# Optimization experiments

Measured on AMD Instinct MI355X. Metric: run time of the kernel, lower is better.

The kernel has to match this reference:

```python
import jax, jax.numpy as jnp
import numpy as np

B, L, C = 16, 450, 768
MID = 256
K = 8912
TEMP = 0.07
ENT_TEMP = 0.01
EPS_NORM = 1e-12


def _l2norm(v):
    n = jnp.sqrt(jnp.sum(v * v, axis=-1, keepdims=True))
    return v / jnp.maximum(n, EPS_NORM)


def setup_inputs() -> dict:
    key = jax.random.key(0)
    k1, k2, k3, k4 = jax.random.split(key, 4)
    x = jax.random.normal(k1, (B, L, C), dtype=jnp.float32)
    W_down = jax.random.normal(k2, (C, MID), dtype=jnp.float32) * (1.0 / np.sqrt(C))
    b_down = jnp.zeros((MID,), dtype=jnp.float32)
    bound = 1.0 / np.sqrt(MID)
    embedding = jax.random.uniform(k3, (K, MID), dtype=jnp.float32, minval=-bound, maxval=bound)
    return {"x": x, "W_down": W_down, "b_down": b_down, "embedding": embedding}


def reference(x, W_down, b_down, embedding):
    Bx, Lx, Cx = x.shape
    # down projection: [B,L,C] -> [B,L,MID]
    z = jnp.einsum('blc,cm->blm', x, W_down) + b_down
    zf = z.reshape(Bx * Lx, MID)
    zn = _l2norm(zf)                       # [N, MID]
    en = _l2norm(embedding)                # [K, MID]
    # squared euclidean distance on the unit sphere: ||a-b||^2 = 2 - 2 a.b
    d = 2.0 - 2.0 * jnp.einsum('nm,km->nk', zn, en)   # [N, K]
    idx = jnp.argmin(d, axis=1)            # [N]
    # codebook usage (no-grad stats)
    occ = jnp.bincount(idx, length=K)
    code_book_usage = jnp.mean((occ > 0).astype(jnp.float32))
    # soft assignment probs (hard_quant branch)
    logits = -d / TEMP
    probs = jax.nn.softmax(logits, axis=1)
    z_q = en[idx]                          # [N, MID]
    vq_loss = jnp.mean((z_q - jax.lax.stop_gradient(zn)) ** 2)
    commit_loss = jnp.mean((jax.lax.stop_gradient(z_q) - zn) ** 2)
    # straight-through estimator
    z_q_ste = zn + jax.lax.stop_gradient(z_q - zn)
    # entropy loss on affinity = -d at entropy temperature
    fa = -d / ENT_TEMP
    p = jax.nn.softmax(fa, axis=-1)
    lp = jax.nn.log_softmax(fa, axis=-1)
    avg_probs = jnp.mean(p, axis=0)
    avg_entropy = -jnp.sum(avg_probs * jnp.log(avg_probs + 1e-5))
    sample_entropy = -jnp.mean(jnp.sum(p * lp, axis=-1))
    entropy_loss = sample_entropy - avg_entropy
    return (z_q_ste.reshape(Bx, Lx, MID), probs.reshape(Bx, Lx, K),
            code_book_usage, vq_loss, commit_loss, entropy_loss)
```

## Files before the change

### kernel.cpp

```cpp
#include <hip/hip_runtime.h>
#include <stdint.h>

#define N_TOK 7200
#define N_PAD 7232
#define N_PAD_A 7296
#define K_CODE 8912
#define K_PAD 8960
#define N_KT 140
#define NKT128 70
#define NMT128 57
#define MID 256
#define C_DIM 768
#define INV_TEMP (1.0f/0.07f)
#define INV_ETEMP 100.0f
#define MARGIN 0.02f
#define CAND_CAP 64
#define EPS_N 1e-12f

typedef __attribute__((ext_vector_type(8))) short short8;
typedef __attribute__((ext_vector_type(4))) float f32x4;

__device__ __forceinline__ unsigned short f2bf(float f) {
    unsigned u = __float_as_uint(f);
    u += 0x7fffu + ((u >> 16) & 1u);
    return (unsigned short)(u >> 16);
}
__device__ __forceinline__ float bf2f(unsigned short h) {
    return __uint_as_float(((unsigned)h) << 16);
}

__device__ __forceinline__ void gload16(const void* g, void* l) {
    __builtin_amdgcn_global_load_lds(
        (const __attribute__((address_space(1))) unsigned int*)g,
        (__attribute__((address_space(3))) unsigned int*)l,
        16, 0, 0);
}

__global__ void k_init(float* ap_acc, int* used, float* acc4, int* ccnt,
                       unsigned short* zn_h, unsigned short* en_h) {
    int i = blockIdx.x * 256 + threadIdx.x;
    if (i < K_CODE) { ap_acc[i] = 0.f; used[i] = 0; }
    if (i < N_TOK) ccnt[i] = 0;
    if (i < 4) acc4[i] = 0.f;
    for (int j = i; j < (N_PAD_A - N_TOK) * MID; j += 8960) zn_h[(size_t)N_TOK * MID + j] = 0;
    for (int j = i; j < (K_PAD - K_CODE) * MID; j += 8960) en_h[(size_t)K_CODE * MID + j] = 0;
}

__global__ void k_wsplit(const float* __restrict__ W,
                         unsigned short* __restrict__ wt_h,
                         unsigned short* __restrict__ wt_l) {
    int i = blockIdx.x * 256 + threadIdx.x;
    if (i >= C_DIM * MID) return;
    int c = i / MID, t = i % MID;
    float v = W[i];
    unsigned short h = f2bf(v);
    unsigned short l = f2bf(v - bf2f(h));
    wt_h[t * C_DIM + c] = h;
    wt_l[t * C_DIM + c] = l;
}

__global__ void k_ennorm(const float* __restrict__ emb,
                         float* __restrict__ en,
                         unsigned short* __restrict__ en_h) {
    int n = blockIdx.x, t = threadIdx.x;
    float v = emb[n * MID + t];
    __shared__ float sb[256];
    sb[t] = v * v; __syncthreads();
    for (int s = 128; s > 0; s >>= 1) { if (t < s) sb[t] += sb[t + s]; __syncthreads(); }
    float nn = sqrtf(sb[0]);
    float o = v / fmaxf(nn, EPS_N);
    en[n * MID + t] = o;
    en_h[n * MID + t] = f2bf(o);
}

__global__ __launch_bounds__(256) void k_zgemm(const float* __restrict__ x,
                                               const unsigned short* __restrict__ wt_h,
                                               const unsigned short* __restrict__ wt_l,
                                               float* __restrict__ zbuf) {
    __shared__ unsigned short ls[4 * 64 * 72];
    unsigned short* xh = ls;
    unsigned short* xl = ls + 64 * 72;
    unsigned short* wh = ls + 2 * 64 * 72;
    unsigned short* wl = ls + 3 * 64 * 72;
    int tid = threadIdx.x;
    int m0 = blockIdx.y * 64;
    int t0 = blockIdx.x * 64;
    int lane = tid & 63, wv = tid >> 6;
    int quad = lane >> 4, l15 = lane & 15;
    int mrow0 = (wv >> 1) * 32, ncol0 = (wv & 1) * 32;
    f32x4 acc[2][2] = {};

    for (int ch = 0; ch < 12; ch++) {
        int c0 = ch * 64;
        for (int it = 0; it < 4; it++) {
            int r = it * 16 + (tid >> 4);
            int cq = tid & 15;
            float4 v = make_float4(0.f, 0.f, 0.f, 0.f);
            int gr = m0 + r;
            if (gr < N_TOK) v = ((const float4*)x)[(size_t)gr * (C_DIM / 4) + (c0 >> 2) + cq];
            unsigned short h0 = f2bf(v.x), h1 = f2bf(v.y), h2 = f2bf(v.z), h3 = f2bf(v.w);
            ushort4 hh = make_ushort4(h0, h1, h2, h3);
            ushort4 ll = make_ushort4(f2bf(v.x - bf2f(h0)), f2bf(v.y - bf2f(h1)),
                                      f2bf(v.z - bf2f(h2)), f2bf(v.w - bf2f(h3)));
            *((ushort4*)&xh[r * 72 + cq * 4]) = hh;
            *((ushort4*)&xl[r * 72 + cq * 4]) = ll;
        }
        for (int it = 0; it < 2; it++) {
            int r = it * 32 + (tid >> 3);
            int cq = tid & 7;
            uint4 vh = ((const uint4*)wt_h)[(size_t)(t0 + r) * (C_DIM / 8) + (c0 >> 3) + cq];
            uint4 vl = ((const uint4*)wt_l)[(size_t)(t0 + r) * (C_DIM / 8) + (c0 >> 3) + cq];
            *((uint4*)&wh[r * 72 + cq * 8]) = vh;
            *((uint4*)&wl[r * 72 + cq * 8]) = vl;
        }
        __syncthreads();
        for (int ks = 0; ks < 2; ks++) {
            int co = ks * 32 + quad * 8;
            short8 ah0 = *((const short8*)&xh[(mrow0 + l15) * 72 + co]);
            short8 ah1 = *((const short8*)&xh[(mrow0 + 16 + l15) * 72 + co]);
            short8 al0 = *((const short8*)&xl[(mrow0 + l15) * 72 + co]);
            short8 al1 = *((const short8*)&xl[(mrow0 + 16 + l15) * 72 + co]);
            short8 bh0 = *((const short8*)&wh[(ncol0 + l15) * 72 + co]);
            short8 bh1 = *((const short8*)&wh[(ncol0 + 16 + l15) * 72 + co]);
            short8 bl0 = *((const short8*)&wl[(ncol0 + l15) * 72 + co]);
            short8 bl1 = *((const short8*)&wl[(ncol0 + 16 + l15) * 72 + co]);
            acc[0][0] = __builtin_amdgcn_mfma_f32_16x16x32_bf16(ah0, bh0, acc[0][0], 0, 0, 0);
            acc[0][1] = __builtin_amdgcn_mfma_f32_16x16x32_bf16(ah0, bh1, acc[0][1], 0, 0, 0);
            acc[1][0] = __builtin_amdgcn_mfma_f32_16x16x32_bf16(ah1, bh0, acc[1][0], 0, 0, 0);
            acc[1][1] = __builtin_amdgcn_mfma_f32_16x16x32_bf16(ah1, bh1, acc[1][1], 0, 0, 0);
            acc[0][0] = __builtin_amdgcn_mfma_f32_16x16x32_bf16(ah0, bl0, acc[0][0], 0, 0, 0);
            acc[0][1] = __builtin_amdgcn_mfma_f32_16x16x32_bf16(ah0, bl1, acc[0][1], 0, 0, 0);
            acc[1][0] = __builtin_amdgcn_mfma_f32_16x16x32_bf16(ah1, bl0, acc[1][0], 0, 0, 0);
            acc[1][1] = __builtin_amdgcn_mfma_f32_16x16x32_bf16(ah1, bl1, acc[1][1], 0, 0, 0);
            acc[0][0] = __builtin_amdgcn_mfma_f32_16x16x32_bf16(al0, bh0, acc[0][0], 0, 0, 0);
            acc[0][1] = __builtin_amdgcn_mfma_f32_16x16x32_bf16(al0, bh1, acc[0][1], 0, 0, 0);
            acc[1][0] = __builtin_amdgcn_mfma_f32_16x16x32_bf16(al1, bh0, acc[1][0], 0, 0, 0);
            acc[1][1] = __builtin_amdgcn_mfma_f32_16x16x32_bf16(al1, bh1, acc[1][1], 0, 0, 0);
        }
        __syncthreads();
    }
    for (int i = 0; i < 2; i++)
        for (int j = 0; j < 2; j++)
            for (int r = 0; r < 4; r++) {
                int gr = m0 + mrow0 + i * 16 + quad * 4 + r;
                int gc = t0 + ncol0 + j * 16 + l15;
                if (gr < N_TOK) zbuf[(size_t)gr * MID + gc] = acc[i][j][r];
            }
}

__global__ void k_znorm(float* __restrict__ zbuf, const float* __restrict__ b_down,
                        unsigned short* __restrict__ zn_h) {
    int n = blockIdx.x, t = threadIdx.x;
    float v = zbuf[(size_t)n * MID + t] + b_down[t];
    __shared__ float sb[256];
    sb[t] = v * v; __syncthreads();
    for (int s = 128; s > 0; s >>= 1) { if (t < s) sb[t] += sb[t + s]; __syncthreads(); }
    float nn = sqrtf(sb[0]);
    float o = v / fmaxf(nn, EPS_N);
    zbuf[(size_t)n * MID + t] = o;
    zn_h[(size_t)n * MID + t] = f2bf(o);
}

template<int PASS>
__global__ __launch_bounds__(256) void k_dpass(const unsigned short* __restrict__ zn_h,
                                               const unsigned short* __restrict__ en_h,
                                               float4* __restrict__ part4,
                                               const float* __restrict__ rs_m,
                                               const float* __restrict__ rs_ist,
                                               const float* __restrict__ rs_is1,
                                               float* __restrict__ ap_acc,
                                               float* __restrict__ out1,
                                               int* __restrict__ ccnt,
                                               int* __restrict__ cand) {
    __shared__ __align__(16) unsigned short lds[2 * 128 * 64];
    unsigned short* lA = lds;
    unsigned short* lB = lds + 128 * 64;
    int tid = threadIdx.x;
    int kt = blockIdx.x, mt = blockIdx.y;
    int m0 = mt * 128, k0 = kt * 128;
    int lane = tid & 63, wv = tid >> 6;
    int quad = lane >> 4, l15 = lane & 15;
    int wr = wv >> 1, wc = wv & 1;
    f32x4 acc[4][4] = {};

    int sr = tid >> 3;
    int scb = (tid & 7) * 16;

    for (int step = 0; step < 4; step++) {
        int cB = step * 128;
        #pragma unroll
        for (int it = 0; it < 4; it++) {
            int r = it * 32 + sr;
            int srcb = scb ^ ((r & 7) << 4);
            const char* gA = (const char*)zn_h + (size_t)(m0 + r) * 512 + cB + srcb;
            const char* gB = (const char*)en_h + (size_t)(k0 + r) * 512 + cB + srcb;
            gload16(gA, (char*)lA + it * 4096 + wv * 1024);
            gload16(gB, (char*)lB + it * 4096 + wv * 1024);
        }
        __syncthreads();
        #pragma unroll
        for (int ks = 0; ks < 2; ks++) {
            short8 a[4], b[4];
            #pragma unroll
            for (int i = 0; i < 4; i++) {
                int ra = wr * 64 + i * 16 + l15;
                int ca = (ks * 64 + quad * 16) ^ ((ra & 7) << 4);
                a[i] = *(const short8*)((const char*)lA + ra * 128 + ca);
                int rb = wc * 64 + i * 16 + l15;
                int cb2 = (ks * 64 + quad * 16) ^ ((rb & 7) << 4);
                b[i] = *(const short8*)((const char*)lB + rb * 128 + cb2);
            }
            #pragma unroll
            for (int i = 0; i < 4; i++)
                #pragma unroll
                for (int j = 0; j < 4; j++)
                    acc[i][j] = __builtin_amdgcn_mfma_f32_16x16x32_bf16(a[i], b[j], acc[i][j], 0, 0, 0);
        }
        __syncthreads();
    }

    if (PASS == 1) {
        int kth = kt * 2 + wc;
        #pragma unroll
        for (int i = 0; i < 4; i++) {
            #pragma unroll
            for (int r = 0; r < 4; r++) {
                float dv[4]; float vmin = 1e30f;
                #pragma unroll
                for (int j = 0; j < 4; j++) {
                    int gc = k0 + wc * 64 + j * 16 + l15;
                    float d = 2.f - 2.f * acc[i][j][r];
                    dv[j] = (gc < K_CODE) ? d : 1e30f;
                    vmin = fminf(vmin, dv[j]);
                }
                vmin = fminf(vmin, __shfl_xor(vmin, 1));
                vmin = fminf(vmin, __shfl_xor(vmin, 2));
                vmin = fminf(vmin, __shfl_xor(vmin, 4));
                vmin = fminf(vmin, __shfl_xor(vmin, 8));
                float st = 0.f, s1 = 0.f, s2 = 0.f;
                #pragma unroll
                for (int j = 0; j < 4; j++) {
                    float dd = vmin - dv[j];
                    st += __expf(dd * INV_TEMP);
                    float te = dd * INV_ETEMP;
                    float e = __expf(te);
                    s1 += e; s2 += e * te;
                }
                st += __shfl_xor(st, 1); st += __shfl_xor(st, 2);
                st += __shfl_xor(st, 4); st += __shfl_xor(st, 8);
                s1 += __shfl_xor(s1, 1); s1 += __shfl_xor(s1, 2);
                s1 += __shfl_xor(s1, 4); s1 += __shfl_xor(s1, 8);
                s2 += __shfl_xor(s2, 1); s2 += __shfl_xor(s2, 2);
                s2 += __shfl_xor(s2, 4); s2 += __shfl_xor(s2, 8);
                if (l15 == 0) {
                    int gr = m0 + wr * 64 + i * 16 + quad * 4 + r;
                    if (gr < N_TOK) part4[(size_t)gr * N_KT + kth] = make_float4(vmin, st, s1, s2);
                }
            }
        }
    } else {
        float* lm = (float*)lds;
        float* lt_ = lm + 128;
        float* l1_ = lt_ + 128;
        float* colacc = l1_ + 128;
        if (tid < 128) {
            int gr = m0 + tid;
            bool ok = gr < N_TOK;
            lm[tid]  = ok ? rs_m[gr]   : 0.f;
            lt_[tid] = ok ? rs_ist[gr] : 0.f;
            l1_[tid] = ok ? rs_is1[gr] : 0.f;
        }
        __syncthreads();
        float ce[4] = {0.f, 0.f, 0.f, 0.f};
        #pragma unroll
        for (int i = 0; i < 4; i++) {
            #pragma unroll
            for (int r = 0; r < 4; r++) {
                int lr = wr * 64 + i * 16 + quad * 4 + r;
                int gr = m0 + lr;
                float m_ = lm[lr], t_ = lt_[lr], i1 = l1_[lr];
                bool okr = gr < N_TOK;
                float thr = m_ + MARGIN;
                #pragma unroll
                for (int j = 0; j < 4; j++) {
                    int gc = k0 + wc * 64 + j * 16 + l15;
                    if (okr && gc < K_CODE) {
                        float d = 2.f - 2.f * acc[i][j][r];
                        ce[j] += __expf((m_ - d) * INV_ETEMP) * i1;
                        float p = __expf((m_ - d) * INV_TEMP) * t_;
                        out1[(size_t)gr * K_CODE + gc] = p;
                        if (d <= thr) {
                            int pd = atomicAdd(&ccnt[gr], 1);
                            if (pd < CAND_CAP) cand[gr * CAND_CAP + pd] = gc;
                        }
                    }
                }
            }
        }
        #pragma unroll
        for (int j = 0; j < 4; j++) {
            ce[j] += __shfl_xor(ce[j], 16);
            ce[j] += __shfl_xor(ce[j], 32);
        }
        if (quad == 0) {
            #pragma unroll
            for (int j = 0; j < 4; j++)
                colacc[wr * 128 + wc * 64 + j * 16 + l15] = ce[j];
        }
        __syncthreads();
        if (tid < 128) {
            int gc = k0 + tid;
            if (gc < K_CODE) atomicAdd(&ap_acc[gc], colacc[tid] + colacc[128 + tid]);
        }
    }
}

__global__ void k_combine(const float4* __restrict__ part4,
                          float* __restrict__ rs_m, float* __restrict__ rs_ist,
                          float* __restrict__ rs_is1,
                          float* __restrict__ acc4) {
    int sub = threadIdx.x >> 6;
    int row = blockIdx.x * 4 + sub;
    int l = threadIdx.x & 63;
    float4 pv[3];
    float m = 1e30f;
    #pragma unroll
    for (int c = 0; c < 3; c++) {
        int t = l + c * 64;
        pv[c] = (t < N_KT) ? part4[(size_t)row * N_KT + t] : make_float4(1e30f, 0.f, 0.f, 0.f);
        m = fminf(m, pv[c].x);
    }
    #pragma unroll
    for (int s = 1; s < 64; s <<= 1) m = fminf(m, __shfl_xor(m, s));
    float st = 0.f, s1 = 0.f, s2 = 0.f;
    #pragma unroll
    for (int c = 0; c < 3; c++) {
        float mb = pv[c].x;
        int t = l + c * 64;
        if (t < N_KT && mb < 1e29f) {
            float dT = (m - mb) * INV_TEMP;
            st += __expf(dT) * pv[c].y;
            float dE = (m - mb) * INV_ETEMP;
            float e = __expf(dE);
            s1 += e * pv[c].z;
            s2 += e * (pv[c].w + dE * pv[c].z);
        }
    }
    #pragma unroll
    for (int s = 1; s < 64; s <<= 1) {
        st += __shfl_xor(st, s);
        s1 += __shfl_xor(s1, s);
        s2 += __shfl_xor(s2, s);
    }
    if (l == 0) {
        rs_m[row] = m;
        rs_ist[row] = 1.f / st;
        rs_is1[row] = 1.f / s1;
        atomicAdd(&acc4[1], s2 / s1 - __logf(s1));
    }
}

__global__ void k_refine(const float* __restrict__ zn, const float* __restrict__ en,
                         const int* __restrict__ ccnt, const int* __restrict__ cand,
                         int* __restrict__ idxb, int* __restrict__ used,
                         float* __restrict__ acc4) {
    int n = blockIdx.x * 4 + (threadIdx.x >> 6);
    int lane = threadIdx.x & 63;
    if (n >= N_TOK) return;
    int cnt = ccnt[n];
    if (cnt > CAND_CAP) cnt = CAND_CAP;
    float4 a = ((const float4*)(zn + (size_t)n * MID))[lane];
    float best = 1e30f; int bj = K_CODE;
    for (int c = 0; c < cnt; c++) {
        int code = cand[n * CAND_CAP + c];
        float4 b = ((const float4*)(en + (size_t)code * MID))[lane];
        float s = a.x * b.x + a.y * b.y + a.z * b.z + a.w * b.w;
        #pragma unroll
        for (int off = 1; off < 64; off <<= 1) s += __shfl_xor(s, off);
        float dist = 2.f - 2.f * s;
        if (dist < best || (dist == best && code < bj)) { best = dist; bj = code; }
    }
    float4 b = ((const float4*)(en + (size_t)bj * MID))[lane];
    float dx = b.x - a.x, dy = b.y - a.y, dz = b.z - a.z, dw = b.w - a.w;
    float sq = dx * dx + dy * dy + dz * dz + dw * dw;
    #pragma unroll
    for (int off = 32; off > 0; off >>= 1) sq += __shfl_down(sq, off);
    if (lane == 0) {
        idxb[n] = bj;
        used[bj] = 1;
        atomicAdd(&acc4[0], sq);
    }
}

__global__ void k_out0(const float* __restrict__ en, const int* __restrict__ idxb,
                       float* __restrict__ out0) {
    int n = blockIdx.x, t = threadIdx.x;
    int j = idxb[n];
    out0[(size_t)n * MID + t] = en[(size_t)j * MID + t];
}

__global__ void k_scal(const int* __restrict__ used, const float* __restrict__ ap_acc,
                       const float* __restrict__ acc4, float* __restrict__ outs) {
    int t = threadIdx.x;
    float uSum = 0.f, aeSum = 0.f;
    for (int k = t; k < K_CODE; k += 256) {
        uSum += (float)used[k];
        float ap = ap_acc[k] * (1.0f / (float)N_TOK);
        aeSum += ap * __logf(ap + 1e-5f);
    }
    __shared__ float sb[256];
    sb[t] = uSum; __syncthreads();
    for (int s = 128; s > 0; s >>= 1) { if (t < s) sb[t] += sb[t + s]; __syncthreads(); }
    uSum = sb[0];
    __syncthreads(); sb[t] = aeSum; __syncthreads();
    for (int s = 128; s > 0; s >>= 1) { if (t < s) sb[t] += sb[t + s]; __syncthreads(); }
    aeSum = sb[0];
    if (t == 0) {
        outs[0] = uSum / (float)K_CODE;
        float vq = acc4[0] / (float)((size_t)N_TOK * MID);
        outs[1] = vq;
        outs[2] = vq;
        outs[3] = -(acc4[1] / (float)N_TOK) + aeSum;
    }
}

extern "C" void kernel_launch(void* const* d_in, const int* in_sizes, int n_in,
                              void* d_out, int out_size, void* d_ws, size_t ws_size,
                              hipStream_t stream) {
    const float* x   = (const float*)d_in[0];
    const float* W   = (const float*)d_in[1];
    const float* b   = (const float*)d_in[2];
    const float* emb = (const float*)d_in[3];

    float* out  = (float*)d_out;
    float* out0 = out;
    float* out1 = out + (size_t)N_TOK * MID;
    float* outs = out + (size_t)N_TOK * MID + (size_t)N_TOK * K_CODE;

    char* w = (char*)d_ws;
    size_t off = 0;
    auto carve = [&](size_t bytes) { void* p = w + off; off += (bytes + 255) & ~(size_t)255; return p; };
    float*          zn    = (float*)         carve((size_t)N_PAD * MID * 4);
    float*          en    = (float*)         carve((size_t)K_PAD * MID * 4);
    unsigned short* zn_h  = (unsigned short*)carve((size_t)N_PAD_A * MID * 2);
    unsigned short* en_h  = (unsigned short*)carve((size_t)K_PAD * MID * 2);
    unsigned short* wt_h  = (unsigned short*)carve((size_t)MID * C_DIM * 2);
    unsigned short* wt_l  = (unsigned short*)carve((size_t)MID * C_DIM * 2);
    float4*         part4 = (float4*)        carve((size_t)N_TOK * N_KT * 16);
    float*          rs_m  = (float*)         carve((size_t)N_TOK * 4);
    float*          rs_ist= (float*)         carve((size_t)N_TOK * 4);
    float*          rs_is1= (float*)         carve((size_t)N_TOK * 4);
    int*            ccnt  = (int*)           carve((size_t)N_TOK * 4);
    int*            cand  = (int*)           carve((size_t)N_TOK * CAND_CAP * 4);
    int*            idxb  = (int*)           carve((size_t)N_TOK * 4);
    float*          ap_acc= (float*)         carve((size_t)K_CODE * 4);
    int*            used  = (int*)           carve((size_t)K_CODE * 4);
    float*          acc4  = (float*)         carve(16);
    (void)ws_size; (void)in_sizes; (void)n_in; (void)out_size;

    k_init   <<<35, 256, 0, stream>>>(ap_acc, used, acc4, ccnt, zn_h, en_h);
    k_wsplit <<<(C_DIM * MID + 255) / 256, 256, 0, stream>>>(W, wt_h, wt_l);
    k_ennorm <<<K_CODE, 256, 0, stream>>>(emb, en, en_h);
    k_zgemm  <<<dim3(4, 113), 256, 0, stream>>>(x, wt_h, wt_l, zn);
    k_znorm  <<<N_TOK, 256, 0, stream>>>(zn, b, zn_h);
    k_dpass<1><<<dim3(NKT128, NMT128), 256, 0, stream>>>(zn_h, en_h, part4, rs_m, rs_ist, rs_is1, ap_acc, out1, ccnt, cand);
    k_combine<<<N_TOK / 4, 256, 0, stream>>>(part4, rs_m, rs_ist, rs_is1, acc4);
    k_dpass<2><<<dim3(NKT128, NMT128), 256, 0, stream>>>(zn_h, en_h, part4, rs_m, rs_ist, rs_is1, ap_acc, out1, ccnt, cand);
    k_refine <<<N_TOK / 4, 256, 0, stream>>>(zn, en, ccnt, cand, idxb, used, acc4);
    k_out0   <<<N_TOK, 256, 0, stream>>>(en, idxb, out0);
    k_scal   <<<1, 256, 0, stream>>>(used, ap_acc, acc4, outs);
}
```

Before: 682.8 us.

## Fuse prep kernels, double-buffer dpass LDS, remap blocks per XCD, fold out0

Merges the init, weight-split and codebook-normalize kernels into one launch and folds the gather of z_q into the refine kernel, which removes two launches and a reread of the index buffer. The distance-pass GEMM now double-buffers its LDS tiles so the next K-step's global-to-LDS loads are issued before the current step's MFMAs. Workgroup IDs are remapped so that consecutive tiles land on the same XCD, aiming at better L2 reuse. LDS use per block doubles to 64KB, which may lower occupancy.

```diff
diff --git a/kernel.cpp b/kernel.cpp
--- a/kernel.cpp
+++ b/kernel.cpp
@@ -36,41 +36,39 @@
         16, 0, 0);
 }
 
-__global__ void k_init(float* ap_acc, int* used, float* acc4, int* ccnt,
-                       unsigned short* zn_h, unsigned short* en_h) {
-    int i = blockIdx.x * 256 + threadIdx.x;
-    if (i < K_CODE) { ap_acc[i] = 0.f; used[i] = 0; }
-    if (i < N_TOK) ccnt[i] = 0;
-    if (i < 4) acc4[i] = 0.f;
-    for (int j = i; j < (N_PAD_A - N_TOK) * MID; j += 8960) zn_h[(size_t)N_TOK * MID + j] = 0;
-    for (int j = i; j < (K_PAD - K_CODE) * MID; j += 8960) en_h[(size_t)K_CODE * MID + j] = 0;
-}
-
-__global__ void k_wsplit(const float* __restrict__ W,
-                         unsigned short* __restrict__ wt_h,
-                         unsigned short* __restrict__ wt_l) {
-    int i = blockIdx.x * 256 + threadIdx.x;
-    if (i >= C_DIM * MID) return;
-    int c = i / MID, t = i % MID;
-    float v = W[i];
-    unsigned short h = f2bf(v);
-    unsigned short l = f2bf(v - bf2f(h));
-    wt_h[t * C_DIM + c] = h;
-    wt_l[t * C_DIM + c] = l;
-}
-
-__global__ void k_ennorm(const float* __restrict__ emb,
-                         float* __restrict__ en,
-                         unsigned short* __restrict__ en_h) {
-    int n = blockIdx.x, t = threadIdx.x;
-    float v = emb[n * MID + t];
+__global__ void k_prep(const float* __restrict__ emb,
+                       float* __restrict__ en, unsigned short* __restrict__ en_h,
+                       const float* __restrict__ W,
+                       unsigned short* __restrict__ wt_h, unsigned short* __restrict__ wt_l,
+                       float* __restrict__ ap_acc, int* __restrict__ used,
+                       float* __restrict__ acc4, int* __restrict__ ccnt,
+                       unsigned short* __restrict__ zn_h) {
     __shared__ float sb[256];
-    sb[t] = v * v; __syncthreads();
-    for (int s = 128; s > 0; s >>= 1) { if (t < s) sb[t] += sb[t + s]; __syncthreads(); }
-    float nn = sqrtf(sb[0]);
-    float o = v / fmaxf(nn, EPS_N);
-    en[n * MID + t] = o;
-    en_h[n * MID + t] = f2bf(o);
+    int b = blockIdx.x, t = threadIdx.x;
+    if (b < K_CODE) {
+        float v = emb[b * MID + t];
+        sb[t] = v * v; __syncthreads();
+        for (int s = 128; s > 0; s >>= 1) { if (t < s) sb[t] += sb[t + s]; __syncthreads(); }
+        float nn = sqrtf(sb[0]);
+        float o = v / fmaxf(nn, EPS_N);
+        en[b * MID + t] = o;
+        en_h[b * MID + t] = f2bf(o);
+    } else if (b < K_CODE + 768) {
+        int i = (b - K_CODE) * 256 + t;
+        int c = i / MID, tc = i % MID;
+        float v = W[i];
+        unsigned short h = f2bf(v);
+        unsigned short l = f2bf(v - bf2f(h));
+        wt_h[tc * C_DIM + c] = h;
+        wt_l[tc * C_DIM + c] = l;
+    } else {
+        int i = (b - K_CODE - 768) * 256 + t;
+        if (i < K_CODE) { ap_acc[i] = 0.f; used[i] = 0; }
+        if (i < N_TOK) ccnt[i] = 0;
+        if (i < 4) acc4[i] = 0.f;
+        for (int j = i; j < (N_PAD_A - N_TOK) * MID; j += 8960) zn_h[(size_t)N_TOK * MID + j] = 0;
+        for (int j = i; j < (K_PAD - K_CODE) * MID; j += 8960) en_h[(size_t)K_CODE * MID + j] = 0;
+    }
 }
 
 __global__ __launch_bounds__(256) void k_zgemm(const float* __restrict__ x,
@@ -172,11 +170,16 @@
                                                float* __restrict__ out1,
                                                int* __restrict__ ccnt,
                                                int* __restrict__ cand) {
-    __shared__ __align__(16) unsigned short lds[2 * 128 * 64];
-    unsigned short* lA = lds;
-    unsigned short* lB = lds + 128 * 64;
+    __shared__ __align__(16) char lds[2 * 32768];
     int tid = threadIdx.x;
-    int kt = blockIdx.x, mt = blockIdx.y;
+    {
+    }
+    int flat = blockIdx.x * NMT128 + blockIdx.y;
+    const int NW = NKT128 * NMT128;
+    const int q = NW >> 3, r8 = NW & 7;
+    int xcd = flat & 7, sidx = flat >> 3;
+    int wg = (xcd < r8 ? xcd * (q + 1) : r8 * (q + 1) + (xcd - r8) * q) + sidx;
+    int kt = wg / NMT128, mt = wg - kt * NMT128;
     int m0 = mt * 128, k0 = kt * 128;
     int lane = tid & 63, wv = tid >> 6;
     int quad = lane >> 4, l15 = lane & 15;
@@ -186,18 +189,27 @@
     int sr = tid >> 3;
     int scb = (tid & 7) * 16;
 
-    for (int step = 0; step < 4; step++) {
+    auto stage = [&](int step, int buf) {
         int cB = step * 128;
+        char* base = lds + buf * 32768;
         #pragma unroll
         for (int it = 0; it < 4; it++) {
             int r = it * 32 + sr;
             int srcb = scb ^ ((r & 7) << 4);
-            const char* gA = (const char*)zn_h + (size_t)(m0 + r) * 512 + cB + srcb;
-            const char* gB = (const char*)en_h + (size_t)(k0 + r) * 512 + cB + srcb;
-            gload16(gA, (char*)lA + it * 4096 + wv * 1024);
-            gload16(gB, (char*)lB + it * 4096 + wv * 1024);
-        }
-        __syncthreads();
+            gload16((const char*)zn_h + (size_t)(m0 + r) * 512 + cB + srcb,
+                    base + it * 4096 + wv * 1024);
+            gload16((const char*)en_h + (size_t)(k0 + r) * 512 + cB + srcb,
+                    base + 16384 + it * 4096 + wv * 1024);
+        }
+    };
+
+    stage(0, 0);
+    __syncthreads();
+    int cur = 0;
+    for (int step = 0; step < 4; step++) {
+        if (step < 3) stage(step + 1, cur ^ 1);
+        const char* lA = lds + cur * 32768;
+        const char* lB = lA + 16384;
         #pragma unroll
         for (int ks = 0; ks < 2; ks++) {
             short8 a[4], b[4];
@@ -205,10 +217,10 @@
             for (int i = 0; i < 4; i++) {
                 int ra = wr * 64 + i * 16 + l15;
                 int ca = (ks * 64 + quad * 16) ^ ((ra & 7) << 4);
-                a[i] = *(const short8*)((const char*)lA + ra * 128 + ca);
+                a[i] = *(const short8*)(lA + ra * 128 + ca);
                 int rb = wc * 64 + i * 16 + l15;
                 int cb2 = (ks * 64 + quad * 16) ^ ((rb & 7) << 4);
-                b[i] = *(const short8*)((const char*)lB + rb * 128 + cb2);
+                b[i] = *(const short8*)(lB + rb * 128 + cb2);
             }
             #pragma unroll
             for (int i = 0; i < 4; i++)
@@ -217,6 +229,7 @@
                     acc[i][j] = __builtin_amdgcn_mfma_f32_16x16x32_bf16(a[i], b[j], acc[i][j], 0, 0, 0);
         }
         __syncthreads();
+        cur ^= 1;
     }
 
     if (PASS == 1) {
@@ -363,7 +376,7 @@
 __global__ void k_refine(const float* __restrict__ zn, const float* __restrict__ en,
                          const int* __restrict__ ccnt, const int* __restrict__ cand,
                          int* __restrict__ idxb, int* __restrict__ used,
-                         float* __restrict__ acc4) {
+                         float* __restrict__ acc4, float* __restrict__ out0) {
     int n = blockIdx.x * 4 + (threadIdx.x >> 6);
     int lane = threadIdx.x & 63;
     if (n >= N_TOK) return;
@@ -381,6 +394,7 @@
         if (dist < best || (dist == best && code < bj)) { best = dist; bj = code; }
     }
     float4 b = ((const float4*)(en + (size_t)bj * MID))[lane];
+    ((float4*)(out0 + (size_t)n * MID))[lane] = b;
     float dx = b.x - a.x, dy = b.y - a.y, dz = b.z - a.z, dw = b.w - a.w;
     float sq = dx * dx + dy * dy + dz * dz + dw * dw;
     #pragma unroll
@@ -390,13 +404,6 @@
         used[bj] = 1;
         atomicAdd(&acc4[0], sq);
     }
-}
-
-__global__ void k_out0(const float* __restrict__ en, const int* __restrict__ idxb,
-                       float* __restrict__ out0) {
-    int n = blockIdx.x, t = threadIdx.x;
-    int j = idxb[n];
-    out0[(size_t)n * MID + t] = en[(size_t)j * MID + t];
 }
 
 __global__ void k_scal(const int* __restrict__ used, const float* __restrict__ ap_acc,
@@ -458,15 +465,13 @@
     float*          acc4  = (float*)         carve(16);
     (void)ws_size; (void)in_sizes; (void)n_in; (void)out_size;
 
-    k_init   <<<35, 256, 0, stream>>>(ap_acc, used, acc4, ccnt, zn_h, en_h);
-    k_wsplit <<<(C_DIM * MID + 255) / 256, 256, 0, stream>>>(W, wt_h, wt_l);
-    k_ennorm <<<K_CODE, 256, 0, stream>>>(emb, en, en_h);
+    k_prep   <<<K_CODE + 768 + 35, 256, 0, stream>>>(emb, en, en_h, W, wt_h, wt_l,
+                                                     ap_acc, used, acc4, ccnt, zn_h);
     k_zgemm  <<<dim3(4, 113), 256, 0, stream>>>(x, wt_h, wt_l, zn);
     k_znorm  <<<N_TOK, 256, 0, stream>>>(zn, b, zn_h);
     k_dpass<1><<<dim3(NKT128, NMT128), 256, 0, stream>>>(zn_h, en_h, part4, rs_m, rs_ist, rs_is1, ap_acc, out1, ccnt, cand);
     k_combine<<<N_TOK / 4, 256, 0, stream>>>(part4, rs_m, rs_ist, rs_is1, acc4);
     k_dpass<2><<<dim3(NKT128, NMT128), 256, 0, stream>>>(zn_h, en_h, part4, rs_m, rs_ist, rs_is1, ap_acc, out1, ccnt, cand);
-    k_refine <<<N_TOK / 4, 256, 0, stream>>>(zn, en, ccnt, cand, idxb, used, acc4);
-    k_out0   <<<N_TOK, 256, 0, stream>>>(en, idxb, out0);
+    k_refine <<<N_TOK / 4, 256, 0, stream>>>(zn, en, ccnt, cand, idxb, used, acc4, out0);
     k_scal   <<<1, 256, 0, stream>>>(used, ap_acc, acc4, outs);
 }
```

Result: slower. 708.5 us (+3.8%).
